# Optimization experiments

Measured on AMD Instinct MI355X. Metric: run time of the kernel, lower is better.

The kernel has to match this reference:

```python
import jax, jax.numpy as jnp
import numpy as np

N_E = 512
E_DIM = 128
LEGACY = 0.2
B, T = 64, 1024


def setup_inputs() -> dict:
    key = jax.random.key(0)
    k1, k2 = jax.random.split(key, 2)
    key_soft = jax.random.normal(k1, (B, T, E_DIM), dtype=jnp.float32)
    emb_weight = jax.random.uniform(k2, (N_E + 1, E_DIM), dtype=jnp.float32,
                                    minval=-1.0 / N_E, maxval=1.0 / N_E)
    zero_ts_mask = jnp.zeros((B,), dtype=jnp.bool_)
    return {"key_soft": key_soft, "emb_weight": emb_weight, "zero_ts_mask": zero_ts_mask}


def _neighbor_indices(d, zero_ts_mask, n_e):
    # d: [B, T, n_e+1] (no grad needed; only used for int index selection)
    ind0 = jnp.clip(jnp.argmin(d[:, 0, :], axis=1), 0, n_e - 1)
    ind0 = jnp.where(zero_ts_mask, 0, ind0)

    def step(ind, d_t):  # ind: [B], d_t: [B, n_e+1]
        d_here = jnp.take_along_axis(d_t, ind[:, None], axis=1)[:, 0]
        ind_next = jnp.clip(ind + 1, 0, n_e - 1)
        d_next = jnp.take_along_axis(d_t, ind_next[:, None], axis=1)[:, 0]
        ind_new = jnp.where(d_here <= d_next, ind, ind_next)
        return ind_new, ind_new

    _, rest = jax.lax.scan(step, ind0, jnp.swapaxes(d[:, 1:, :], 0, 1))  # [T-1, B]
    return jnp.concatenate([ind0[None, :], rest], axis=0).T  # [B, T]


def reference(key_soft, emb_weight, zero_ts_mask):
    sg = jax.lax.stop_gradient
    n_e = emb_weight.shape[0] - 1
    b, t, e_dim = key_soft.shape

    # squared-distance matrix: [B, T, n_e+1]
    d = (jnp.sum(key_soft ** 2, axis=-1, keepdims=True)
         + jnp.sum(emb_weight ** 2, axis=1)
         - 2.0 * jnp.einsum('btd,nd->btn', key_soft, emb_weight))
    d_ng = sg(d)

    min_indices = jnp.argmin(d_ng, axis=-1)                 # [B, T] (over full n_e+1)
    enc = _neighbor_indices(d_ng, zero_ts_mask, n_e)        # [B, T]

    key_hard_here = emb_weight[enc]                                  # [B, T, D]
    key_hard_next = emb_weight[jnp.clip(enc + 1, 0, n_e - 1)]        # [B, T, D]
    key_min = emb_weight[min_indices]                                # [B, T, D]

    def vq_loss(kh):
        return (jnp.sum((sg(key_soft) - kh) ** 2, axis=-1)
                + jnp.sum((key_soft - sg(kh)) ** 2, axis=-1) * LEGACY)

    loss_here_base = vq_loss(key_hard_here)
    loss_next_base = vq_loss(key_hard_next)

    energy = (jnp.sum((sg(key_soft) - key_hard_next) ** 2, axis=-1)
              - jnp.sum((sg(key_soft) - key_hard_here) ** 2, axis=-1)
              + (jnp.sum((key_soft - sg(key_hard_next)) ** 2, axis=-1)
                 - jnp.sum((key_soft - sg(key_hard_here)) ** 2, axis=-1)) * LEGACY)

    change = (enc[:, 1:] - enc[:, :-1]) != 0
    same_hard_mask = jnp.where(change, 0.0, 1.0)
    energy_change = (energy[:, 1:] - energy[:, :-1]) * same_hard_mask
    loss_energy_descent = jnp.maximum(energy_change + 1e-06 / n_e,
                                      jnp.zeros_like(energy_change)).mean()
    energy_mean = energy.mean()

    loss_min_indices = vq_loss(key_min)
    loss_min_here = jnp.where(loss_min_indices < loss_here_base, loss_min_indices, 0.0)
    loss_min_next = jnp.where(loss_min_indices < loss_next_base, loss_min_indices, 0.0)

    loss_here = loss_here_base - loss_next_base - loss_min_here
    loss_next = loss_next_base - loss_here_base - loss_min_next

    key_hard = key_soft + sg(key_hard_here - key_soft)  # straight-through

    v = jnp.max(jnp.max(enc, axis=1) - jnp.min(enc, axis=1))
    return (key_hard, enc, v, loss_here, loss_next, energy_mean, loss_energy_descent)
```

## Files before the change

### kernel.cpp

```cpp
#include <hip/hip_runtime.h>
#include <cfloat>
#include <cstdint>

#define B_  64
#define T_  1024
#define D_  128
#define NE  512
#define P_  (B_*T_)

#define O_KH   0
#define O_ENC  (P_*D_)
#define O_V    (O_ENC + P_)
#define O_LH   (O_V + 1)
#define O_LN   (O_LH + P_)
#define O_EM   (O_LN + P_)
#define O_LED  (O_EM + 1)

typedef __attribute__((ext_vector_type(8))) short bf16x8;
typedef __attribute__((ext_vector_type(4))) float floatx4;
typedef unsigned long long u64;

__device__ __forceinline__ void pack8(const float4& a, const float4& b,
                                      uint4& h, uint4& l)
{
    float v[8] = {a.x,a.y,a.z,a.w,b.x,b.y,b.z,b.w};
    unsigned hw[4], lw[4];
    #pragma unroll
    for (int e = 0; e < 4; e++) {
        const unsigned ua = __float_as_uint(v[2*e]);
        const unsigned ub = __float_as_uint(v[2*e+1]);
        const float fa = __uint_as_float(ua & 0xffff0000u);
        const float fb = __uint_as_float(ub & 0xffff0000u);
        const unsigned da = __float_as_uint(v[2*e]   - fa);
        const unsigned db = __float_as_uint(v[2*e+1] - fb);
        hw[e] = (ub & 0xffff0000u) | (ua >> 16);
        lw[e] = (db & 0xffff0000u) | (da >> 16);
    }
    h = make_uint4(hw[0],hw[1],hw[2],hw[3]);
    l = make_uint4(lw[0],lw[1],lw[2],lw[3]);
}

__device__ __forceinline__ u64 shflx64(u64 v, int d)
{
    const int lo = __shfl_xor((int)(unsigned)(v & 0xffffffffULL), d);
    const int hi = __shfl_xor((int)(unsigned)(v >> 32), d);
    return ((u64)(unsigned)hi << 32) | (unsigned)lo;
}

__device__ __forceinline__ unsigned sortkey(float f)
{
    const unsigned b = __float_as_uint(f);
    return b ^ (unsigned)(((int)b >> 31) | (int)0x80000000);
}

__global__ __launch_bounds__(256) void kFG(const float* __restrict__ emb,
                                           unsigned short* __restrict__ ehi,
                                           unsigned short* __restrict__ elo,
                                           float* __restrict__ sq)
{
    const int t = blockIdx.x * 256 + threadIdx.x;
    const int n = t >> 2, kst = t & 3;
    const float4* src = (const float4*)(emb + (size_t)n * D_ + kst * 32);
    float ss = 0.f;
    #pragma unroll
    for (int g = 0; g < 4; g++) {
        const float4 a = src[2*g], b = src[2*g+1];
        ss += a.x*a.x + a.y*a.y + a.z*a.z + a.w*a.w
            + b.x*b.x + b.y*b.y + b.z*b.z + b.w*b.w;
        uint4 h, l;
        pack8(a, b, h, l);
        const int f = ((n >> 4) * 4 + kst) * 4 + g;
        *(uint4*)(ehi + (size_t)f*128 + (size_t)(n & 15)*8) = h;
        *(uint4*)(elo + (size_t)f*128 + (size_t)(n & 15)*8) = l;
    }
    ss += __shfl_xor(ss, 1);
    ss += __shfl_xor(ss, 2);
    if (kst == 0) sq[n] = ss;
}

__global__ __launch_bounds__(256) void kA(const float* __restrict__ ks,
                                          const float* __restrict__ sq,
                                          const unsigned short* __restrict__ ehi,
                                          const unsigned short* __restrict__ elo,
                                          u64* __restrict__ bits,
                                          float* __restrict__ sfirst,
                                          float* __restrict__ slast,
                                          unsigned* __restrict__ mins,
                                          unsigned short* __restrict__ mini16)
{
    __shared__ unsigned short Bh[64*128];
    __shared__ unsigned short Bl[64*128];

    const int tid  = threadIdx.x;
    const int lane = tid & 63;
    const int wv   = tid >> 6;
    const int m    = lane & 15;
    const int q    = lane >> 4;
    const int pt   = blockIdx.x & 1023;
    const int p0   = pt * 64;
    const int ch   = (blockIdx.x >> 10) * 4 + wv;
    const int nb   = ch * 64;

    {
        const int srow = tid >> 2;
        const int scg  = tid & 3;
        const float4* sp = (const float4*)(ks + ((size_t)p0 + srow)*D_ + scg*32);
        #pragma unroll
        for (int g = 0; g < 4; g++) {
            uint4 h, l;
            pack8(sp[2*g], sp[2*g+1], h, l);
            const int cb = (srow*256 + scg*64 + g*16) ^ ((srow & 7) << 4);
            *(uint4*)((char*)Bh + cb) = h;
            *(uint4*)((char*)Bl + cb) = l;
        }
    }
    __syncthreads();

    floatx4 acc[4][4];
    #pragma unroll
    for (int i = 0; i < 4; i++)
        #pragma unroll
        for (int j = 0; j < 4; j++)
            #pragma unroll
            for (int r = 0; r < 4; r++) acc[i][j][r] = 0.f;

    bf16x8 ah[4], al[4], bh[4], bl[4];

    auto loadA = [&](int kst) {
        #pragma unroll
        for (int i = 0; i < 4; i++) {
            const int off = (((ch*4 + i) * 4 + kst) * 4 + q) * 128 + m*8;
            ah[i] = *(const bf16x8*)(ehi + off);
            al[i] = *(const bf16x8*)(elo + off);
        }
    };
    auto loadB = [&](int kst) {
        #pragma unroll
        for (int j = 0; j < 4; j++) {
            const int row = j*16 + m;
            const int cb = (row*256 + kst*64 + q*16) ^ ((row & 7) << 4);
            bh[j] = *(const bf16x8*)((const char*)Bh + cb);
            bl[j] = *(const bf16x8*)((const char*)Bl + cb);
        }
    };
    auto mfma3 = [&]() {
        #pragma unroll
        for (int i = 0; i < 4; i++)
            #pragma unroll
            for (int j = 0; j < 4; j++)
                acc[i][j] = __builtin_amdgcn_mfma_f32_16x16x32_bf16(ah[i], bh[j], acc[i][j], 0, 0, 0);
        #pragma unroll
        for (int i = 0; i < 4; i++)
            #pragma unroll
            for (int j = 0; j < 4; j++)
                acc[i][j] = __builtin_amdgcn_mfma_f32_16x16x32_bf16(ah[i], bl[j], acc[i][j], 0, 0, 0);
        #pragma unroll
        for (int i = 0; i < 4; i++)
            #pragma unroll
            for (int j = 0; j < 4; j++)
                acc[i][j] = __builtin_amdgcn_mfma_f32_16x16x32_bf16(al[i], bh[j], acc[i][j], 0, 0, 0);
    };

    #pragma unroll
    for (int kst = 0; kst < 4; kst++) {
        loadA(kst);
        loadB(kst);
        mfma3();
    }

    float sa[4][4];
    #pragma unroll
    for (int i = 0; i < 4; i++) {
        const float4 s4 = *(const float4*)(sq + nb + i*16 + q*4);
        sa[i][0]=s4.x; sa[i][1]=s4.y; sa[i][2]=s4.z; sa[i][3]=s4.w;
    }
    #pragma unroll
    for (int j = 0; j < 4; j++) {
        float S[4][4];
        #pragma unroll
        for (int i = 0; i < 4; i++)
            #pragma unroll
            for (int r = 0; r < 4; r++)
                S[i][r] = fmaf(-2.f, acc[i][j][r], sa[i][r]);

        float nq[4], ni[4];
        #pragma unroll
        for (int i = 0; i < 4; i++) nq[i] = __shfl_down(S[i][0], 16);
        #pragma unroll
        for (int i = 0; i < 3; i++) ni[i] = __shfl(S[i+1][0], m);
        ni[3] = 0.f;

        u64 w = 0;
        #pragma unroll
        for (int i = 0; i < 4; i++) {
            #pragma unroll
            for (int r = 0; r < 3; r++)
                w |= (u64)(S[i][r] <= S[i][r+1]) << (16*i + 4*q + r);
            if (!(i == 3 && q == 3)) {
                const float nxt = (q < 3) ? nq[i] : ni[i];
                w |= (u64)(S[i][3] <= nxt) << (16*i + 4*q + 3);
            }
        }
        if (ch == 7 && q == 3) w |= 1ULL << 63;
        w |= shflx64(w, 16);
        w |= shflx64(w, 32);

        float mv = S[0][0]; int mi_ = nb + q*4;
        #pragma unroll
        for (int i = 0; i < 4; i++)
            #pragma unroll
            for (int r = 0; r < 4; r++) {
                if (i == 0 && r == 0) continue;
                const int nid = nb + 16*i + 4*q + r;
                if (S[i][r] < mv) { mv = S[i][r]; mi_ = nid; }
            }
        #pragma unroll
        for (int d = 16; d <= 32; d <<= 1) {
            const float v2 = __shfl_xor(mv, d);
            const int   i2 = __shfl_xor(mi_, d);
            if (v2 < mv || (v2 == mv && i2 < mi_)) { mv = v2; mi_ = i2; }
        }

        const size_t pg = (size_t)(p0 + j*16 + m);
        if (q == 0) {
            bits  [pg*8 + ch] = w;
            sfirst[pg*8 + ch] = S[0][0];
            mins  [pg*8 + ch] = sortkey(mv);
            mini16[pg*8 + ch] = (unsigned short)mi_;
        }
        if (q == 3) slast[pg*8 + ch] = S[3][3];
    }
}

struct KBwin { u64 W[8]; float F[8]; float L[8]; };

__global__ __launch_bounds__(64) void kB(const float* __restrict__ ks,
                                         const float* __restrict__ emb,
                                         const unsigned char* __restrict__ mask,
                                         const u64* __restrict__ bits,
                                         const float* __restrict__ sfirst,
                                         const float* __restrict__ slast,
                                         const unsigned* __restrict__ mins,
                                         const unsigned short* __restrict__ mini16,
                                         int* __restrict__ enci,
                                         float* __restrict__ out)
{
    const int b    = blockIdx.x;
    const int lane = threadIdx.x;
    const size_t p0 = (size_t)b * T_;

    const float2 e = ((const float2*)(emb + (size_t)512*D_))[lane];
    const float2 k = ((const float2*)(ks  + p0*D_))[lane];
    float s5 = e.x*(e.x - 2.f*k.x) + e.y*(e.y - 2.f*k.y);
    #pragma unroll
    for (int m = 32; m >= 1; m >>= 1) s5 += __shfl_xor(s5, m);

    u64 kk = ~0ULL;
    if (lane < 8)       kk = ((u64)mins[p0*8 + lane] << 32) | (u64)mini16[p0*8 + lane];
    else if (lane == 8) kk = ((u64)sortkey(s5) << 32) | 512ULL;
    #pragma unroll
    for (int d = 1; d <= 8; d <<= 1) {
        const u64 o = shflx64(kk, d);
        kk = (o < kk) ? o : kk;
    }
    const int mi = __shfl((int)(unsigned)(kk & 0xffffffffULL), 0);
    int cur = (mi < NE) ? mi : NE - 1;
    if (mask[b]) cur = 0;
    if (lane == 0) { enci[p0] = cur; out[O_ENC + p0] = (float)cur; }

    KBwin wa, wb;

    auto loadwin = [&](KBwin& d, int t0) {
        const int t = t0 + lane;
        if (t < T_) {
            const ulonglong2* bp = (const ulonglong2*)(bits + (p0 + t)*8);
            const ulonglong2 w01 = bp[0], w23 = bp[1], w45 = bp[2], w67 = bp[3];
            d.W[0]=w01.x; d.W[1]=w01.y; d.W[2]=w23.x; d.W[3]=w23.y;
            d.W[4]=w45.x; d.W[5]=w45.y; d.W[6]=w67.x; d.W[7]=w67.y;
            const float4* fp = (const float4*)(sfirst + (p0 + t)*8);
            const float4 f0 = fp[0], f1 = fp[1];
            d.F[0]=f0.x; d.F[1]=f0.y; d.F[2]=f0.z; d.F[3]=f0.w;
            d.F[4]=f1.x; d.F[5]=f1.y; d.F[6]=f1.z; d.F[7]=f1.w;
            const float4* lp = (const float4*)(slast + (p0 + t)*8);
            const float4 l0 = lp[0], l1 = lp[1];
            d.L[0]=l0.x; d.L[1]=l0.y; d.L[2]=l0.z; d.L[3]=l0.w;
            d.L[4]=l1.x; d.L[5]=l1.y; d.L[6]=l1.z; d.L[7]=l1.w;
        } else {
            #pragma unroll
            for (int c = 0; c < 8; c++) { d.W[c] = ~0ULL; d.F[c] = 1.f; d.L[c] = 0.f; }
        }
    };

    auto scanwin = [&](KBwin& d, int t0) {
        #pragma unroll
        for (int c = 0; c < 7; c++)
            d.W[c] |= (u64)(d.L[c] <= d.F[c+1]) << 63;

        const int w0   = cur >> 6;
        const int off0 = cur & 63;
        u64 a = d.W[0];
        #pragma unroll
        for (int c = 1; c < 8; c++) a = (w0 == c) ? d.W[c] : a;
        u64 bn = ~0ULL;
        #pragma unroll
        for (int c = 1; c < 8; c++) bn = (w0 == c-1) ? d.W[c] : bn;
        const u64 u = (off0 == 0) ? a : ((a >> off0) | (bn << (64 - off0)));

        const unsigned ulo = (unsigned)u;
        const unsigned uhi = (unsigned)(u >> 32);
        int doff = 0;
        int myenc = cur;
        #pragma unroll
        for (int j = 0; j < 64; j++) {
            const unsigned slo = (unsigned)__builtin_amdgcn_readlane((int)ulo, j);
            const unsigned shi = (unsigned)__builtin_amdgcn_readlane((int)uhi, j);
            const u64 word = ((u64)shi << 32) | slo;
            const int bit = (int)((word >> doff) & 1ULL);
            doff += 1 - bit;
            if (lane == j) myenc = cur + doff;
        }
        cur += doff;
        const int t = t0 + lane;
        if (t < T_) {
            enci[p0 + t] = myenc;
            out[O_ENC + p0 + t] = (float)myenc;
        }
    };

    loadwin(wa, 1);
    #pragma unroll 1
    for (int wp = 0; wp < 8; wp++) {
        const int t0a = 1 + wp*128;
        loadwin(wb, t0a + 64);
        scanwin(wa, t0a);
        if (wp < 7) loadwin(wa, t0a + 128);
        scanwin(wb, t0a + 64);
    }
}

__global__ __launch_bounds__(256) void kC(const float* __restrict__ ks,
                                          const float* __restrict__ emb,
                                          const int* __restrict__ enci,
                                          const unsigned* __restrict__ mins,
                                          const unsigned short* __restrict__ mini16,
                                          float* __restrict__ out,
                                          float* __restrict__ energy)
{
    const int lane = threadIdx.x & 63;
    const size_t p = (size_t)blockIdx.x * 4 + (threadIdx.x >> 6);
    const int q  = lane >> 4;
    const int qm = lane & 15;

    const int eh = enci[p];
    const int en = (eh + 1 < NE) ? eh + 1 : NE - 1;
    const int row = (q == 0) ? eh : ((q == 1) ? en : 512);

    const float4* ksp = (const float4*)(ks + p*D_);
    const float4 k1 = ksp[qm*2], k2 = ksp[qm*2 + 1];
    const float4* ep = (const float4*)(emb + (size_t)row*D_);
    const float4 e1 = ep[qm*2], e2 = ep[qm*2 + 1];

    float d;
    if (q == 3) {
        d = k1.x*k1.x + k1.y*k1.y + k1.z*k1.z + k1.w*k1.w
          + k2.x*k2.x + k2.y*k2.y + k2.z*k2.z + k2.w*k2.w;
    } else {
        d = e1.x*(e1.x - 2.f*k1.x) + e1.y*(e1.y - 2.f*k1.y)
          + e1.z*(e1.z - 2.f*k1.z) + e1.w*(e1.w - 2.f*k1.w)
          + e2.x*(e2.x - 2.f*k2.x) + e2.y*(e2.y - 2.f*k2.y)
          + e2.z*(e2.z - 2.f*k2.z) + e2.w*(e2.w - 2.f*k2.w);
    }
    #pragma unroll
    for (int s = 1; s <= 8; s <<= 1) d += __shfl_xor(d, s);

    const float ph  = __shfl(d, 0);
    const float pn  = __shfl(d, 16);
    const float p5  = __shfl(d, 32);
    const float sqk = __shfl(d, 48);

    u64 kk = ~0ULL;
    if (lane < 8)       kk = ((u64)mins[p*8 + lane] << 32) | (u64)mini16[p*8 + lane];
    else if (lane == 8) kk = ((u64)sortkey(p5) << 32) | 512ULL;
    #pragma unroll
    for (int s = 1; s <= 8; s <<= 1) {
        const u64 o = shflx64(kk, s);
        kk = (o < kk) ? o : kk;
    }
    const int mi = __shfl((int)(unsigned)(kk & 0xffffffffULL), 0);

    float pm;
    if (mi == eh)      pm = ph;
    else if (mi == en) pm = pn;
    else if (mi == 512) pm = p5;
    else {
        const float4* mp = (const float4*)(emb + (size_t)mi*D_);
        const float4 m1 = mp[qm*2], m2 = mp[qm*2 + 1];
        float dm = m1.x*(m1.x - 2.f*k1.x) + m1.y*(m1.y - 2.f*k1.y)
                 + m1.z*(m1.z - 2.f*k1.z) + m1.w*(m1.w - 2.f*k1.w)
                 + m2.x*(m2.x - 2.f*k2.x) + m2.y*(m2.y - 2.f*k2.y)
                 + m2.z*(m2.z - 2.f*k2.z) + m2.w*(m2.w - 2.f*k2.w);
        #pragma unroll
        for (int s = 1; s <= 8; s <<= 1) dm += __shfl_xor(dm, s);
        pm = __shfl(dm, 0);
    }

    if (q == 0) {
        float4 o1, o2;
        o1.x = k1.x + (e1.x - k1.x); o1.y = k1.y + (e1.y - k1.y);
        o1.z = k1.z + (e1.z - k1.z); o1.w = k1.w + (e1.w - k1.w);
        o2.x = k2.x + (e2.x - k2.x); o2.y = k2.y + (e2.y - k2.y);
        o2.z = k2.z + (e2.z - k2.z); o2.w = k2.w + (e2.w - k2.w);
        ((float4*)(out + p*D_))[qm*2]     = o1;
        ((float4*)(out + p*D_))[qm*2 + 1] = o2;
    }

    if (lane == 0) {
        const float lh = 1.2f * (sqk + ph);
        const float ln = 1.2f * (sqk + pn);
        const float lm = 1.2f * (sqk + pm);
        out[O_LH + p] = lh - ln - ((pm < ph) ? lm : 0.f);
        out[O_LN + p] = ln - lh - ((pm < pn) ? lm : 0.f);
        energy[p] = 1.2f * (pn - ph);
    }
}

__global__ __launch_bounds__(256) void kD1(const float* __restrict__ energy,
                                           const int* __restrict__ enci,
                                           double2* __restrict__ part)
{
    __shared__ double sA[256], sB[256];
    const int p = blockIdx.x * 256 + threadIdx.x;
    const float e = energy[p];
    double se = (double)e;
    double sl = 0.0;
    if ((p & (T_-1)) < T_-1) {
        const float ec = (enci[p+1] == enci[p]) ? (energy[p+1] - e) : 0.f;
        sl = (double)fmaxf(ec + (float)(1e-6/512.0), 0.f);
    }
    sA[threadIdx.x] = se; sB[threadIdx.x] = sl;
    __syncthreads();
    for (int s = 128; s >= 1; s >>= 1) {
        if (threadIdx.x < (unsigned)s) {
            sA[threadIdx.x] += sA[threadIdx.x+s];
            sB[threadIdx.x] += sB[threadIdx.x+s];
        }
        __syncthreads();
    }
    if (threadIdx.x == 0) { part[blockIdx.x] = make_double2(sA[0], sB[0]); }
}

__global__ __launch_bounds__(256) void kD2(const double2* __restrict__ part,
                                           const int* __restrict__ enci,
                                           float* __restrict__ out)
{
    __shared__ double sA[256], sB[256];
    const double2 pv = part[threadIdx.x];
    sA[threadIdx.x] = pv.x; sB[threadIdx.x] = pv.y;
    __syncthreads();
    for (int s = 128; s >= 1; s >>= 1) {
        if (threadIdx.x < (unsigned)s) {
            sA[threadIdx.x] += sA[threadIdx.x+s];
            sB[threadIdx.x] += sB[threadIdx.x+s];
        }
        __syncthreads();
    }
    if (threadIdx.x < 64) {
        int v = enci[(size_t)threadIdx.x*T_ + T_-1] - enci[(size_t)threadIdx.x*T_];
        #pragma unroll
        for (int m = 32; m >= 1; m >>= 1) {
            const int v2 = __shfl_xor(v, m);
            v = (v2 > v) ? v2 : v;
        }
        if (threadIdx.x == 0) {
            out[O_V]   = (float)v;
            out[O_EM]  = (float)(sA[0] / (double)P_);
            out[O_LED] = (float)(sB[0] / (double)(B_*(T_-1)));
        }
    }
}

extern "C" void kernel_launch(void* const* d_in, const int* in_sizes, int n_in,
                              void* d_out, int out_size, void* d_ws, size_t ws_size,
                              hipStream_t stream)
{
    const float* ks  = (const float*)d_in[0];
    const float* emb = (const float*)d_in[1];
    const unsigned char* mask = (const unsigned char*)d_in[2];

    float* out = (float*)d_out;
    char* w = (char*)d_ws;
    u64*      bits   = (u64*)     (w);
    float*    sfirst = (float*)   (w + (size_t) 4*1024*1024);
    float*    slast  = (float*)   (w + (size_t) 6*1024*1024);
    unsigned* mins   = (unsigned*)(w + (size_t) 8*1024*1024);
    unsigned short* mini16 = (unsigned short*)(w + (size_t)10*1024*1024);
    int*      enci   = (int*)     (w + (size_t)11*1024*1024);
    float*    energy = (float*)   (w + (size_t)11*1024*1024 + 256*1024);
    float*    sq     = (float*)   (w + (size_t)11*1024*1024 + 512*1024);
    double2*  part   = (double2*) (w + (size_t)11*1024*1024 + 516*1024);
    unsigned short* ehi = (unsigned short*)(w + (size_t)11*1024*1024 + 640*1024);
    unsigned short* elo = (unsigned short*)(w + (size_t)11*1024*1024 + 768*1024);

    kFG<<<8,    256, 0, stream>>>(emb, ehi, elo, sq);
    kA <<<2048, 256, 0, stream>>>(ks, sq, ehi, elo, bits, sfirst, slast, mins, mini16);
    kB <<<B_,   64,  0, stream>>>(ks, emb, mask, bits, sfirst, slast, mins, mini16, enci, out);
    kC <<<P_/4, 256, 0, stream>>>(ks, emb, enci, mins, mini16, out, energy);
    kD1<<<256,  256, 0, stream>>>(energy, enci, part);
    kD2<<<1,    256, 0, stream>>>(part, enci, out);
}
```

Measured before the change: 187.7 us.

## Halve kA position tile for occupancy and fuse final reduction via last-block atomic

kA now processes 32 positions per block instead of 64, doubling the grid to 4096 blocks, halving shared memory and accumulator registers, and adds launch_bounds occupancy hint plus s_setprio around MFMA bursts and hoisted final-stage loads. The final reduction kernel kD2 is folded into kD1 using an atomic counter (reset in kFG) so the last finishing block performs the global reduce. This removes one kernel launch and aims to raise occupancy, at the cost of re-reading embedding fragments twice as often and relying on fence/atomic ordering. The trailing part of kA's epilogue (not shown) must match the 32-row tile for correctness.

```diff
diff --git a/kernel.cpp b/kernel.cpp
--- a/kernel.cpp
+++ b/kernel.cpp
@@ -56,8 +56,10 @@
 __global__ __launch_bounds__(256) void kFG(const float* __restrict__ emb,
                                            unsigned short* __restrict__ ehi,
                                            unsigned short* __restrict__ elo,
-                                           float* __restrict__ sq)
-{
+                                           float* __restrict__ sq,
+                                           unsigned* __restrict__ cnt)
+{
+    if (blockIdx.x == 0 && threadIdx.x == 0) *cnt = 0u;
     const int t = blockIdx.x * 256 + threadIdx.x;
     const int n = t >> 2, kst = t & 3;
     const float4* src = (const float4*)(emb + (size_t)n * D_ + kst * 32);
@@ -78,7 +80,7 @@
     if (kst == 0) sq[n] = ss;
 }
 
-__global__ __launch_bounds__(256) void kA(const float* __restrict__ ks,
+__global__ __launch_bounds__(256, 4) void kA(const float* __restrict__ ks,
                                           const float* __restrict__ sq,
                                           const unsigned short* __restrict__ ehi,
                                           const unsigned short* __restrict__ elo,
@@ -88,43 +90,46 @@
                                           unsigned* __restrict__ mins,
                                           unsigned short* __restrict__ mini16)
 {
-    __shared__ unsigned short Bh[64*128];
-    __shared__ unsigned short Bl[64*128];
+    __shared__ unsigned short Bh[32*128];
+    __shared__ unsigned short Bl[32*128];
 
     const int tid  = threadIdx.x;
     const int lane = tid & 63;
     const int wv   = tid >> 6;
     const int m    = lane & 15;
     const int q    = lane >> 4;
-    const int pt   = blockIdx.x & 1023;
-    const int p0   = pt * 64;
-    const int ch   = (blockIdx.x >> 10) * 4 + wv;
+    const int bid  = blockIdx.x;
+    const int cg   = bid >> 11;
+    const int h    = (bid >> 10) & 1;
+    const int pt   = bid & 1023;
+    const int p0   = pt * 64 + h * 32;
+    const int ch   = cg * 4 + wv;
     const int nb   = ch * 64;
 
     {
-        const int srow = tid >> 2;
-        const int scg  = tid & 3;
-        const float4* sp = (const float4*)(ks + ((size_t)p0 + srow)*D_ + scg*32);
-        #pragma unroll
-        for (int g = 0; g < 4; g++) {
-            uint4 h, l;
-            pack8(sp[2*g], sp[2*g+1], h, l);
-            const int cb = (srow*256 + scg*64 + g*16) ^ ((srow & 7) << 4);
-            *(uint4*)((char*)Bh + cb) = h;
-            *(uint4*)((char*)Bl + cb) = l;
+        const int srow  = tid >> 3;
+        const int spart = tid & 7;
+        const float4* sp = (const float4*)(ks + ((size_t)p0 + srow)*D_ + spart*16);
+        #pragma unroll
+        for (int g = 0; g < 2; g++) {
+            uint4 hh, ll;
+            pack8(sp[2*g], sp[2*g+1], hh, ll);
+            const int cb = (srow*256 + spart*32 + g*16) ^ ((srow & 7) << 4);
+            *(uint4*)((char*)Bh + cb) = hh;
+            *(uint4*)((char*)Bl + cb) = ll;
         }
     }
     __syncthreads();
 
-    floatx4 acc[4][4];
+    floatx4 acc[4][2];
     #pragma unroll
     for (int i = 0; i < 4; i++)
         #pragma unroll
-        for (int j = 0; j < 4; j++)
+        for (int j = 0; j < 2; j++)
             #pragma unroll
             for (int r = 0; r < 4; r++) acc[i][j][r] = 0.f;
 
-    bf16x8 ah[4], al[4], bh[4], bl[4];
+    bf16x8 ah[4], al[4], bh[2], bl[2];
 
     auto loadA = [&](int kst) {
         #pragma unroll
@@ -136,7 +141,7 @@
     };
     auto loadB = [&](int kst) {
         #pragma unroll
-        for (int j = 0; j < 4; j++) {
+        for (int j = 0; j < 2; j++) {
             const int row = j*16 + m;
             const int cb = (row*256 + kst*64 + q*16) ^ ((row & 7) << 4);
             bh[j] = *(const bf16x8*)((const char*)Bh + cb);
@@ -144,38 +149,43 @@
         }
     };
     auto mfma3 = [&]() {
+        __builtin_amdgcn_s_setprio(1);
         #pragma unroll
         for (int i = 0; i < 4; i++)
             #pragma unroll
-            for (int j = 0; j < 4; j++)
+            for (int j = 0; j < 2; j++)
                 acc[i][j] = __builtin_amdgcn_mfma_f32_16x16x32_bf16(ah[i], bh[j], acc[i][j], 0, 0, 0);
         #pragma unroll
         for (int i = 0; i < 4; i++)
             #pragma unroll
-            for (int j = 0; j < 4; j++)
+            for (int j = 0; j < 2; j++)
                 acc[i][j] = __builtin_amdgcn_mfma_f32_16x16x32_bf16(ah[i], bl[j], acc[i][j], 0, 0, 0);
         #pragma unroll
         for (int i = 0; i < 4; i++)
             #pragma unroll
-            for (int j = 0; j < 4; j++)
+            for (int j = 0; j < 2; j++)
                 acc[i][j] = __builtin_amdgcn_mfma_f32_16x16x32_bf16(al[i], bh[j], acc[i][j], 0, 0, 0);
+        __builtin_amdgcn_s_setprio(0);
     };
 
     #pragma unroll
-    for (int kst = 0; kst < 4; kst++) {
+    for (int kst = 0; kst < 3; kst++) {
         loadA(kst);
         loadB(kst);
         mfma3();
     }
-
+    loadA(3);
+    loadB(3);
     float sa[4][4];
     #pragma unroll
     for (int i = 0; i < 4; i++) {
         const float4 s4 = *(const float4*)(sq + nb + i*16 + q*4);
         sa[i][0]=s4.x; sa[i][1]=s4.y; sa[i][2]=s4.z; sa[i][3]=s4.w;
     }
-    #pragma unroll
-    for (int j = 0; j < 4; j++) {
+    mfma3();
+
+    #pragma unroll
+    for (int j = 0; j < 2; j++) {
         float S[4][4];
         #pragma unroll
         for (int i = 0; i < 4; i++)
@@ -426,9 +436,12 @@
 
 __global__ __launch_bounds__(256) void kD1(const float* __restrict__ energy,
                                            const int* __restrict__ enci,
-                                           double2* __restrict__ part)
+                                           double2* __restrict__ part,
+                                           unsigned* __restrict__ cnt,
+                                           float* __restrict__ out)
 {
     __shared__ double sA[256], sB[256];
+    __shared__ unsigned done;
     const int p = blockIdx.x * 256 + threadIdx.x;
     const float e = energy[p];
     double se = (double)e;
@@ -446,16 +459,20 @@
         }
         __syncthreads();
     }
-    if (threadIdx.x == 0) { part[blockIdx.x] = make_double2(sA[0], sB[0]); }
-}
-
-__global__ __launch_bounds__(256) void kD2(const double2* __restrict__ part,
-                                           const int* __restrict__ enci,
-                                           float* __restrict__ out)
-{
-    __shared__ double sA[256], sB[256];
-    const double2 pv = part[threadIdx.x];
-    sA[threadIdx.x] = pv.x; sB[threadIdx.x] = pv.y;
+    if (threadIdx.x == 0) {
+        part[blockIdx.x] = make_double2(sA[0], sB[0]);
+        __threadfence();
+        done = atomicAdd(cnt, 1u);
+    }
+    __syncthreads();
+    if (done != 255u) return;
+
+    __threadfence();
+    double pvx, pvy;
+    pvx = ((volatile double*)part)[2*threadIdx.x];
+    pvy = ((volatile double*)part)[2*threadIdx.x + 1];
+    __syncthreads();
+    sA[threadIdx.x] = pvx; sB[threadIdx.x] = pvy;
     __syncthreads();
     for (int s = 128; s >= 1; s >>= 1) {
         if (threadIdx.x < (unsigned)s) {
@@ -498,13 +515,13 @@
     float*    energy = (float*)   (w + (size_t)11*1024*1024 + 256*1024);
     float*    sq     = (float*)   (w + (size_t)11*1024*1024 + 512*1024);
     double2*  part   = (double2*) (w + (size_t)11*1024*1024 + 516*1024);
+    unsigned* cnt    = (unsigned*)(w + (size_t)11*1024*1024 + 520*1024);
     unsigned short* ehi = (unsigned short*)(w + (size_t)11*1024*1024 + 640*1024);
     unsigned short* elo = (unsigned short*)(w + (size_t)11*1024*1024 + 768*1024);
 
-    kFG<<<8,    256, 0, stream>>>(emb, ehi, elo, sq);
-    kA <<<2048, 256, 0, stream>>>(ks, sq, ehi, elo, bits, sfirst, slast, mins, mini16);
+    kFG<<<8,    256, 0, stream>>>(emb, ehi, elo, sq, cnt);
+    kA <<<4096, 256, 0, stream>>>(ks, sq, ehi, elo, bits, sfirst, slast, mins, mini16);
     kB <<<B_,   64,  0, stream>>>(ks, emb, mask, bits, sfirst, slast, mins, mini16, enci, out);
     kC <<<P_/4, 256, 0, stream>>>(ks, emb, enci, mins, mini16, out, energy);
-    kD1<<<256,  256, 0, stream>>>(energy, enci, part);
-    kD2<<<1,    256, 0, stream>>>(part, enci, out);
-}
+    kD1<<<256,  256, 0, stream>>>(energy, enci, part, cnt, out);
+}
```

Result: no change. 184.2 us (-1.8%).
